# Optimization experiments

Hardware: AMD Instinct MI355X
Metric: run time of the kernel (lower is better)

Reference implementation:

```python
import jax, jax.numpy as jnp
import numpy as np

D = 128        # embed_d
L = 2          # n_layers
B = 4096       # batch of center nodes (drugs)
S = 10         # num_samples per neighbor type (hard-coded in node_het_agg)
NUM_CELLS, NUM_DRUGS, NUM_GENES = 2000, 4000, 20000
DRUG_F, GENE_F = 1024, 2048
NT = 3         # node types: cell, drug, gene


def setup_inputs() -> dict:
    key = jax.random.key(0)
    ks = jax.random.split(key, 16)
    s = 0.02
    inp = {
        # raw per-type feature tables (feature_loader / embedding table)
        "drug_feats": jax.random.normal(ks[0], (NUM_DRUGS, DRUG_F), jnp.float32),
        "gene_feats": jax.random.normal(ks[1], (NUM_GENES, GENE_F), jnp.float32),
        "cell_tab": jax.random.normal(ks[2], (NUM_CELLS, D), jnp.float32) * s,
        # feat_proj linears
        "W_drug": jax.random.normal(ks[3], (DRUG_F, D), jnp.float32) * s,
        "b_drug": jnp.zeros((D,), jnp.float32),
        "W_gene": jax.random.normal(ks[4], (GENE_F, D), jnp.float32) * s,
        "b_gene": jnp.zeros((D,), jnp.float32),
        # RnnGnnLayer params: per layer, per neighbor type, a simple tanh RNN
        "rnn_Wx": jax.random.normal(ks[5], (L, NT, D, D), jnp.float32) * s,
        "rnn_Wh": jax.random.normal(ks[6], (L, NT, D, D), jnp.float32) * s,
        "rnn_b": jnp.zeros((L, NT, D), jnp.float32),
        # per-layer attention vector over [self || candidate]
        "att_w": jax.random.normal(ks[7], (L, 2 * D), jnp.float32) * s,
        # center node ids (drug type) and pre-sampled neighbor ids per layer/type
        "center_ids": jax.random.randint(ks[8], (B,), 0, NUM_DRUGS, jnp.int32),
        "cell_neigh": jax.random.randint(ks[9], (L, B, S), 0, NUM_CELLS, jnp.int32),
        "drug_neigh": jax.random.randint(ks[10], (L, B, S), 0, NUM_DRUGS, jnp.int32),
        "gene_neigh": jax.random.randint(ks[11], (L, B, S), 0, NUM_GENES, jnp.int32),
    }
    return inp


def reference(drug_feats, gene_feats, cell_tab, W_drug, b_drug, W_gene, b_gene,
              rnn_Wx, rnn_Wh, rnn_b, att_w,
              center_ids, cell_neigh, drug_neigh, gene_neigh):
    # conteng_agg per node type: gather raw features then project to embed_d
    def emb_cell(idx):
        return cell_tab[idx]                              # [..., D]

    def emb_drug(idx):
        return drug_feats[idx] @ W_drug + b_drug          # gather [..., DRUG_F] -> [..., D]

    def emb_gene(idx):
        return gene_feats[idx] @ W_gene + b_gene

    def rnn_agg(x, Wx, Wh, b):
        # x: [B, S, D]; simple tanh RNN over the S sampled neighbors, last hidden
        def step(h, xt):
            h = jnp.tanh(xt @ Wx + h @ Wh + b)
            return h, None
        h0 = jnp.zeros((x.shape[0], Wx.shape[1]), x.dtype)
        h_last, _ = jax.lax.scan(step, h0, jnp.swapaxes(x, 0, 1))
        return h_last                                      # [B, D]

    h = emb_drug(center_ids)                               # initial center embeds [B, D]
    n_layers = rnn_Wx.shape[0]
    for l in range(n_layers):
        neigh = [(cell_neigh[l], emb_cell), (drug_neigh[l], emb_drug), (gene_neigh[l], emb_gene)]
        aggs = []
        for t, (idx, emb) in enumerate(neigh):
            x = emb(idx)                                   # [B, S, D]
            aggs.append(rnn_agg(x, rnn_Wx[l, t], rnn_Wh[l, t], rnn_b[l, t]))
        cands = jnp.stack([h] + aggs, axis=1)              # [B, 1+NT, D]
        self_b = jnp.broadcast_to(h[:, None, :], cands.shape)
        scores = jax.nn.leaky_relu(jnp.concatenate([self_b, cands], axis=-1) @ att_w[l])  # [B, 1+NT]
        alpha = jax.nn.softmax(scores, axis=1)
        h = jnp.einsum('bc,bcd->bd', alpha, cands)         # attention-weighted combine
    return h                                               # [B, D]
```

## Files before the change

kernel.cpp:

```cpp
#include <hip/hip_runtime.h>
#include <stdint.h>

#define D 128
#define Ssz 10
#define HP 136

typedef uint16_t u16;
typedef uint32_t u32;
typedef __attribute__((ext_vector_type(8))) short short8;
typedef __attribute__((ext_vector_type(4))) float f32x4;

#define AS1U32(p) ((const __attribute__((address_space(1))) u32*)(p))
#define AS3U32(p) ((__attribute__((address_space(3))) u32*)(p))

__device__ __forceinline__ u16 f2bf(float f){
  u32 x = __float_as_uint(f);
  return (u16)((x + 0x7fffu + ((x >> 16) & 1u)) >> 16);
}
__device__ __forceinline__ float bf2f(u16 u){ return __uint_as_float(((u32)u) << 16); }

__device__ __forceinline__ float ftanh(float x){
  float e = __expf(2.0f * x);
  return 1.0f - 2.0f / (e + 1.0f);
}

__global__ __launch_bounds__(256) void transpose_k(const float* __restrict__ W,
                                                   u16* __restrict__ WT, int K){
  int i = blockIdx.x * 256 + threadIdx.x;
  if (i >= K * D) return;
  int n = i / K, k = i - n * K;
  WT[i] = f2bf(W[k * D + n]);
}

__global__ __launch_bounds__(256) void transpose_b6(const float* __restrict__ W,
                                                    u16* __restrict__ WT){
  int i = blockIdx.x * 256 + threadIdx.x;
  int j = i & 16383, n = j >> 7, k = j & 127;
  WT[i] = f2bf(W[(i & ~16383) + k * D + n]);
}

__global__ __launch_bounds__(256) void cvt_bf16(const float* __restrict__ in,
                                                u16* __restrict__ out, int n2){
  int i = blockIdx.x * 256 + threadIdx.x;
  if (i >= n2) return;
  float v0 = in[2 * i], v1 = in[2 * i + 1];
  ((u32*)out)[i] = (u32)f2bf(v0) | ((u32)f2bf(v1) << 16);
}

__global__ __launch_bounds__(256) void proj_gemm(
    const float* __restrict__ feats, int K, int M,
    const u16* __restrict__ WT,
    const float* __restrict__ bias,
    u16* __restrict__ outb,
    float* __restrict__ outf)
{
  __shared__ u16 Bt[128 * 128];

  int lane = threadIdx.x & 63;
  int wave = threadIdx.x >> 6;
  int quad = lane >> 4, l16 = lane & 15;
  int m0 = blockIdx.x * 64 + wave * 16;

  int row = min(m0 + l16, M - 1);
  const float* aptr = feats + (long)row * K + quad * 8;

  int st_nrow = wave * 32 + (lane >> 4);
  int st_p    = lane & 15;

  f32x4 acc[8];
#pragma unroll
  for (int nt = 0; nt < 8; ++nt){
    float bv = bias[nt * 16 + l16];
    f32x4 t = {bv, bv, bv, bv};
    acc[nt] = t;
  }

  f32x4 afA[4][2], afB[4][2];
#pragma unroll
  for (int ks = 0; ks < 4; ++ks){
    afA[ks][0] = *(const f32x4*)(aptr + ks * 32);
    afA[ks][1] = *(const f32x4*)(aptr + ks * 32 + 4);
  }

  auto chunk_step = [&](f32x4 (&acur)[4][2], f32x4 (&anxt)[4][2], int kc) {
#pragma unroll
    for (int j = 0; j < 8; ++j){
      int n = st_nrow + j * 4;
      int c = st_p ^ (n & 15);
      const u16* g = WT + (long)n * K + kc + c * 8;
      __builtin_amdgcn_global_load_lds(AS1U32(g),
                                       AS3U32(&Bt[(wave * 8 + j) * 512]),
                                       16, 0, 0);
    }
    if (kc + 128 < K){
#pragma unroll
      for (int ks = 0; ks < 4; ++ks){
        anxt[ks][0] = *(const f32x4*)(aptr + kc + 128 + ks * 32);
        anxt[ks][1] = *(const f32x4*)(aptr + kc + 128 + ks * 32 + 4);
      }
    }
    __syncthreads();

#pragma unroll
    for (int ks = 0; ks < 4; ++ks){
      short8 a;
#pragma unroll
      for (int q = 0; q < 4; ++q){
        a[q]     = (short)f2bf(acur[ks][0][q]);
        a[4 + q] = (short)f2bf(acur[ks][1][q]);
      }
#pragma unroll
      for (int nt = 0; nt < 8; ++nt){
        int n = nt * 16 + l16;
        int p = (ks * 4 + quad) ^ l16;
        short8 b = *(const short8*)(&Bt[n * 128 + p * 8]);
        acc[nt] = __builtin_amdgcn_mfma_f32_16x16x32_bf16(a, b, acc[nt], 0, 0, 0);
      }
    }
    __syncthreads();
  };

  for (int kc = 0; kc < K; kc += 256){
    chunk_step(afA, afB, kc);
    chunk_step(afB, afA, kc + 128);
  }

#pragma unroll
  for (int nt = 0; nt < 8; ++nt){
    int col = nt * 16 + l16;
#pragma unroll
    for (int r = 0; r < 4; ++r){
      int mr = m0 + quad * 4 + r;
      if (mr < M){
        long o = (long)mr * D + col;
        if (outb) outb[o] = f2bf(acc[nt][r]);
        if (outf) outf[o] = acc[nt][r];
      }
    }
  }
}

__global__ __launch_bounds__(256) void xw_gemm(
    const u16* __restrict__ cellT, const u16* __restrict__ drugPb,
    const u16* __restrict__ genePb,
    const u16* __restrict__ WxT6,
    const float* __restrict__ bvec,
    float* __restrict__ xwb)
{
  int bx = blockIdx.x, l = blockIdx.y;
  int t, m0, M, rbase;
  const u16* tab;
  if (bx < 32)      { t = 0; m0 = bx * 64;        M = 2000;  rbase = 0;    tab = cellT; }
  else if (bx < 95) { t = 1; m0 = (bx - 32) * 64; M = 4000;  rbase = 2000; tab = drugPb; }
  else              { t = 2; m0 = (bx - 95) * 64; M = 20000; rbase = 6000; tab = genePb; }
  int mat = l * 3 + t;
  const u16* WT = WxT6 + (size_t)mat * 16384;

  int lane = threadIdx.x & 63, wave = threadIdx.x >> 6;
  int quad = lane >> 4, l16 = lane & 15;
  int mt = m0 + wave * 16;
  int mr = min(mt + l16, M - 1);

  short8 a[4];
#pragma unroll
  for (int ks = 0; ks < 4; ++ks)
    a[ks] = *(const short8*)(tab + (long)mr * D + ks * 32 + quad * 8);

  f32x4 acc[8];
#pragma unroll
  for (int nt = 0; nt < 8; ++nt){
    float bv = bvec[mat * D + nt * 16 + l16];
    f32x4 tv = {bv, bv, bv, bv};
    acc[nt] = tv;
  }
#pragma unroll
  for (int nt = 0; nt < 8; ++nt){
#pragma unroll
    for (int ks = 0; ks < 4; ++ks){
      short8 b = *(const short8*)(WT + (nt * 16 + l16) * D + ks * 32 + quad * 8);
      acc[nt] = __builtin_amdgcn_mfma_f32_16x16x32_bf16(a[ks], b, acc[nt], 0, 0, 0);
    }
  }
#pragma unroll
  for (int nt = 0; nt < 8; ++nt){
    int col = nt * 16 + l16;
#pragma unroll
    for (int r = 0; r < 4; ++r){
      int mrow = mt + quad * 4 + r;
      if (mrow < M)
        xwb[((long)l * 26000 + rbase + mrow) * D + col] = acc[nt][r];
    }
  }
}

__global__ __launch_bounds__(256) void gather_f32(
    const float* __restrict__ tab, const int* __restrict__ idx,
    float* __restrict__ out, int nrows, int ntab)
{
  int gt = blockIdx.x * 256 + threadIdx.x;
  int r = gt >> 6, c = gt & 63;
  if (r >= nrows) return;
  int row = min(max(idx[r], 0), ntab - 1);
  ((float2*)out)[(long)r * 64 + c] = ((const float2*)tab)[(long)row * 64 + c];
}

__global__ __launch_bounds__(256, 3) void rnn6_kernel(
    const float* __restrict__ xwb,
    const u16* __restrict__ WhT6,
    const int* __restrict__ cn, const int* __restrict__ dn,
    const int* __restrict__ gn,
    int b0,
    u16* __restrict__ agg, int CB)
{
  __shared__ u16 hbuf[16 * HP];

  int t = blockIdx.y, l = blockIdx.z;
  const int* idx = (t == 0) ? cn : (t == 1) ? dn : gn;
  int rbase = (t == 0) ? 0 : (t == 1) ? 2000 : 6000;
  int nmax  = (t == 0) ? 2000 : (t == 1) ? 4000 : 20000;
  const float* xw = xwb + ((size_t)l * 26000 + rbase) * D;
  const u16* WT = WhT6 + (size_t)(l * 3 + t) * 16384;

  int tid = threadIdx.x, lane = tid & 63, wave = tid >> 6;
  int quad = lane >> 4, l16 = lane & 15;
  int n0 = wave * 32;

  short8 whf[2][4];
#pragma unroll
  for (int nt = 0; nt < 2; ++nt){
    int n = n0 + nt * 16 + l16;
#pragma unroll
    for (int ks = 0; ks < 4; ++ks)
      whf[nt][ks] = *(const short8*)(WT + n * D + ks * 32 + quad * 8);
  }

  for (int i = tid; i < 16 * HP; i += 256) hbuf[i] = 0;

  int brow = blockIdx.x * 16;
  const int* ip = idx + ((size_t)l * 4096 + b0 + brow + quad * 4) * Ssz;
  long arow = ((long)(l * 3 + t) * CB + brow) * D;

  int nidA[4], nidB[4];
  float xwA[8], xwB[8];
#pragma unroll
  for (int r = 0; r < 4; ++r) nidA[r] = min(max(ip[r * Ssz], 0), nmax - 1);
#pragma unroll
  for (int r = 0; r < 4; ++r){
    const float* p = xw + (long)nidA[r] * D + n0 + l16;
    xwA[r] = p[0]; xwA[4 + r] = p[16];
  }
#pragma unroll
  for (int r = 0; r < 4; ++r) nidB[r] = min(max(ip[r * Ssz + 1], 0), nmax - 1);
  __syncthreads();

  auto step = [&](int s, float (&xwc)[8], int (&nidn)[4],
                  float (&xwn)[8], int (&nidf)[4]){
    if (s + 1 < Ssz){
#pragma unroll
      for (int r = 0; r < 4; ++r){
        const float* p = xw + (long)nidn[r] * D + n0 + l16;
        xwn[r] = p[0]; xwn[4 + r] = p[16];
      }
    }
    if (s + 2 < Ssz){
#pragma unroll
      for (int r = 0; r < 4; ++r)
        nidf[r] = min(max(ip[r * Ssz + s + 2], 0), nmax - 1);
    }
    short8 hf[4];
#pragma unroll
    for (int ks = 0; ks < 4; ++ks)
      hf[ks] = *(const short8*)(&hbuf[l16 * HP + ks * 32 + quad * 8]);
    f32x4 acc0 = {xwc[0], xwc[1], xwc[2], xwc[3]};
    f32x4 acc1 = {xwc[4], xwc[5], xwc[6], xwc[7]};
#pragma unroll
    for (int ks = 0; ks < 4; ++ks){
      acc0 = __builtin_amdgcn_mfma_f32_16x16x32_bf16(hf[ks], whf[0][ks], acc0, 0, 0, 0);
      acc1 = __builtin_amdgcn_mfma_f32_16x16x32_bf16(hf[ks], whf[1][ks], acc1, 0, 0, 0);
    }
    __syncthreads();
#pragma unroll
    for (int r = 0; r < 4; ++r){
      float v0 = ftanh(acc0[r]);
      float v1 = ftanh(acc1[r]);
      hbuf[(quad * 4 + r) * HP + n0 + l16]      = f2bf(v0);
      hbuf[(quad * 4 + r) * HP + n0 + 16 + l16] = f2bf(v1);
      if (s == Ssz - 1){
        long o = arow + (long)(quad * 4 + r) * D;
        agg[o + n0 + l16]      = f2bf(v0);
        agg[o + n0 + 16 + l16] = f2bf(v1);
      }
    }
    __syncthreads();
  };

  step(0, xwA, nidB, xwB, nidA);
  step(1, xwB, nidA, xwA, nidB);
  step(2, xwA, nidB, xwB, nidA);
  step(3, xwB, nidA, xwA, nidB);
  step(4, xwA, nidB, xwB, nidA);
  step(5, xwB, nidA, xwA, nidB);
  step(6, xwA, nidB, xwB, nidA);
  step(7, xwB, nidA, xwA, nidB);
  step(8, xwA, nidB, xwB, nidA);
  step(9, xwB, nidA, xwA, nidB);
}

__global__ __launch_bounds__(256) void att_kernel(
    const float* __restrict__ h,
    const u16* __restrict__ agg,
    const float* __restrict__ aw,
    float* __restrict__ out,
    int CB)
{
  int gt = blockIdx.x * 256 + threadIdx.x;
  int lane = gt & 63;
  int b = gt >> 6;
  int e = 2 * lane;

  float c[4][2];
  c[0][0] = h[(long)b * D + e];
  c[0][1] = h[(long)b * D + e + 1];
#pragma unroll
  for (int t = 0; t < 3; ++t){
    c[t + 1][0] = bf2f(agg[((long)t * CB + b) * D + e]);
    c[t + 1][1] = bf2f(agg[((long)t * CB + b) * D + e + 1]);
  }
  float as0 = aw[e],     as1 = aw[e + 1];
  float ac0 = aw[D + e], ac1 = aw[D + e + 1];

  float selfp = c[0][0] * as0 + c[0][1] * as1;
  float sc[4];
#pragma unroll
  for (int cc = 0; cc < 4; ++cc) sc[cc] = selfp + c[cc][0] * ac0 + c[cc][1] * ac1;
#pragma unroll
  for (int off = 32; off >= 1; off >>= 1){
#pragma unroll
    for (int cc = 0; cc < 4; ++cc) sc[cc] += __shfl_xor(sc[cc], off, 64);
  }
#pragma unroll
  for (int cc = 0; cc < 4; ++cc) sc[cc] = sc[cc] > 0.f ? sc[cc] : 0.01f * sc[cc];

  float mx = fmaxf(fmaxf(sc[0], sc[1]), fmaxf(sc[2], sc[3]));
  float ex[4], ssum = 0.f;
#pragma unroll
  for (int cc = 0; cc < 4; ++cc){ ex[cc] = expf(sc[cc] - mx); ssum += ex[cc]; }
  float o0 = 0.f, o1 = 0.f;
#pragma unroll
  for (int cc = 0; cc < 4; ++cc){
    float a = ex[cc] / ssum;
    o0 += a * c[cc][0];
    o1 += a * c[cc][1];
  }
  out[(long)b * D + e]     = o0;
  out[(long)b * D + e + 1] = o1;
}

extern "C" void kernel_launch(void* const* d_in, const int* in_sizes, int n_in,
                              void* d_out, int out_size, void* d_ws, size_t ws_size,
                              hipStream_t stream)
{
  const float* drug_feats = (const float*)d_in[0];
  const float* gene_feats = (const float*)d_in[1];
  const float* cell_tab   = (const float*)d_in[2];
  const float* W_drug     = (const float*)d_in[3];
  const float* b_drug     = (const float*)d_in[4];
  const float* W_gene     = (const float*)d_in[5];
  const float* b_gene     = (const float*)d_in[6];
  const float* rnn_Wx     = (const float*)d_in[7];
  const float* rnn_Wh     = (const float*)d_in[8];
  const float* rnn_b      = (const float*)d_in[9];
  const float* att_w      = (const float*)d_in[10];
  const int* center_ids   = (const int*)d_in[11];
  const int* cell_neigh   = (const int*)d_in[12];
  const int* drug_neigh   = (const int*)d_in[13];
  const int* gene_neigh   = (const int*)d_in[14];

  u16* ws     = (u16*)d_ws;
  u16* WdT    = ws;
  u16* WgT    = WdT + 131072;
  u16* WxT6   = WgT + 262144;
  u16* WhT6   = WxT6 + 98304;
  u16* cellT  = WhT6 + 98304;
  u16* drugPb = cellT + 256000;
  u16* genePb = drugPb + 512000;
  float* drugPf = (float*)(genePb + 2560000);
  float* xwb    = drugPf + 512000;
  u16* agg      = (u16*)(xwb + 6656000);

  int CB = 4096;
  while (CB > 64){
    size_t need = 36507648u + (size_t)1536 * CB;
    if (need <= ws_size) break;
    CB >>= 1;
  }
  float* h = (float*)d_out;

  transpose_k<<<512, 256, 0, stream>>>(W_drug, WdT, 1024);
  transpose_k<<<1024, 256, 0, stream>>>(W_gene, WgT, 2048);
  transpose_b6<<<384, 256, 0, stream>>>(rnn_Wx, WxT6);
  transpose_b6<<<384, 256, 0, stream>>>(rnn_Wh, WhT6);
  cvt_bf16<<<500, 256, 0, stream>>>(cell_tab, cellT, 2000 * 64);

  proj_gemm<<<63, 256, 0, stream>>>(drug_feats, 1024, 4000,
                                    WdT, b_drug, drugPb, drugPf);
  proj_gemm<<<313, 256, 0, stream>>>(gene_feats, 2048, 20000,
                                     WgT, b_gene, genePb, (float*)nullptr);

  xw_gemm<<<dim3(408, 2), 256, 0, stream>>>(cellT, drugPb, genePb,
                                            WxT6, rnn_b, xwb);

  for (int b0 = 0; b0 < 4096; b0 += CB){
    gather_f32<<<CB / 4, 256, 0, stream>>>(drugPf, center_ids + b0,
                                           h + (size_t)b0 * D, CB, 4000);
    rnn6_kernel<<<dim3(CB / 16, 3, 2), 256, 0, stream>>>(
        xwb, WhT6, cell_neigh, drug_neigh, gene_neigh, b0, agg, CB);

    for (int l = 0; l < 2; ++l){
      att_kernel<<<CB / 4, 256, 0, stream>>>(h + (size_t)b0 * D,
                                             agg + (size_t)l * 3 * CB * D,
                                             att_w + (size_t)l * 2 * D,
                                             h + (size_t)b0 * D, CB);
    }
  }
}
```

Before: 366.7 us.

## Fuse prep kernels, projection with Wx GEMM, and gather with attention layers

Merges the five weight/table conversion kernels into one prep kernel. The per-type Wx GEMM now runs inside the projection GEMM epilogue, reusing the accumulator tile from LDS, so the bf16 projected tables are never written or reloaded. The center gather and both attention layers are fused into one kernel, and the workspace-dependent chunking loop is dropped. This cuts launch count and global traffic, but it assumes the workspace can hold the full batch and makes the projection kernel's epilogue longer.

Measured after the change: 360.9 us. No clear change (-1.6%).

```diff
diff --git a/kernel.cpp b/kernel.cpp
--- a/kernel.cpp
+++ b/kernel.cpp
@@ -4,6 +4,7 @@
 #define D 128
 #define Ssz 10
 #define HP 136
+#define NB 4096
 
 typedef uint16_t u16;
 typedef uint32_t u32;
@@ -24,34 +25,47 @@
   return 1.0f - 2.0f / (e + 1.0f);
 }
 
-__global__ __launch_bounds__(256) void transpose_k(const float* __restrict__ W,
-                                                   u16* __restrict__ WT, int K){
+__global__ __launch_bounds__(256) void prep_kernel(
+    const float* __restrict__ W_drug, const float* __restrict__ W_gene,
+    const float* __restrict__ rnn_Wx, const float* __restrict__ rnn_Wh,
+    const float* __restrict__ cell_tab,
+    u16* __restrict__ WdT, u16* __restrict__ WgT,
+    u16* __restrict__ WxT6, u16* __restrict__ WhT6,
+    u16* __restrict__ cellT)
+{
   int i = blockIdx.x * 256 + threadIdx.x;
-  if (i >= K * D) return;
-  int n = i / K, k = i - n * K;
-  WT[i] = f2bf(W[k * D + n]);
-}
-
-__global__ __launch_bounds__(256) void transpose_b6(const float* __restrict__ W,
-                                                    u16* __restrict__ WT){
-  int i = blockIdx.x * 256 + threadIdx.x;
-  int j = i & 16383, n = j >> 7, k = j & 127;
-  WT[i] = f2bf(W[(i & ~16383) + k * D + n]);
-}
-
-__global__ __launch_bounds__(256) void cvt_bf16(const float* __restrict__ in,
-                                                u16* __restrict__ out, int n2){
-  int i = blockIdx.x * 256 + threadIdx.x;
-  if (i >= n2) return;
-  float v0 = in[2 * i], v1 = in[2 * i + 1];
-  ((u32*)out)[i] = (u32)f2bf(v0) | ((u32)f2bf(v1) << 16);
+  if (i < 131072){
+    int n = i >> 10, k = i & 1023;
+    WdT[i] = f2bf(W_drug[k * D + n]);
+  } else if (i < 393216){
+    int j = i - 131072;
+    int n = j >> 11, k = j & 2047;
+    WgT[j] = f2bf(W_gene[k * D + n]);
+  } else if (i < 491520){
+    int j = i - 393216;
+    int n = (j >> 7) & 127, k = j & 127;
+    WxT6[j] = f2bf(rnn_Wx[(j & ~16383) + k * D + n]);
+  } else if (i < 589824){
+    int j = i - 491520;
+    int n = (j >> 7) & 127, k = j & 127;
+    WhT6[j] = f2bf(rnn_Wh[(j & ~16383) + k * D + n]);
+  } else {
+    int j = i - 589824;
+    float v0 = cell_tab[2 * j], v1 = cell_tab[2 * j + 1];
+    ((u32*)cellT)[j] = (u32)f2bf(v0) | ((u32)f2bf(v1) << 16);
+  }
 }
 
 __global__ __launch_bounds__(256) void proj_gemm(
     const float* __restrict__ feats, int K, int M,
     const u16* __restrict__ WT,
     const float* __restrict__ bias,
-    u16* __restrict__ outb,
+    const u16* __restrict__ Wx0,
+    const u16* __restrict__ Wx1,
+    const float* __restrict__ rb0,
+    const float* __restrict__ rb1,
+    float* __restrict__ xw0,
+    float* __restrict__ xw1,
     float* __restrict__ outf)
 {
   __shared__ u16 Bt[128 * 128];
@@ -125,46 +139,80 @@
     chunk_step(afB, afA, kc + 128);
   }
 
-#pragma unroll
-  for (int nt = 0; nt < 8; ++nt){
-    int col = nt * 16 + l16;
-#pragma unroll
-    for (int r = 0; r < 4; ++r){
-      int mr = m0 + quad * 4 + r;
-      if (mr < M){
-        long o = (long)mr * D + col;
-        if (outb) outb[o] = f2bf(acc[nt][r]);
-        if (outf) outf[o] = acc[nt][r];
-      }
-    }
-  }
-}
-
-__global__ __launch_bounds__(256) void xw_gemm(
-    const u16* __restrict__ cellT, const u16* __restrict__ drugPb,
-    const u16* __restrict__ genePb,
+  if (outf){
+#pragma unroll
+    for (int nt = 0; nt < 8; ++nt){
+      int col = nt * 16 + l16;
+#pragma unroll
+      for (int r = 0; r < 4; ++r){
+        int mr = m0 + quad * 4 + r;
+        if (mr < M) outf[(long)mr * D + col] = acc[nt][r];
+      }
+    }
+  }
+
+  u16* Pl = Bt + wave * 2176;
+#pragma unroll
+  for (int nt = 0; nt < 8; ++nt)
+#pragma unroll
+    for (int r = 0; r < 4; ++r)
+      Pl[(quad * 4 + r) * HP + nt * 16 + l16] = f2bf(acc[nt][r]);
+  __syncthreads();
+
+  short8 paf[4];
+#pragma unroll
+  for (int ks = 0; ks < 4; ++ks)
+    paf[ks] = *(const short8*)(&Pl[l16 * HP + ks * 32 + quad * 8]);
+
+  auto xw_pass = [&](const u16* Wx, const float* rb, float* xw){
+    f32x4 ac2[8];
+#pragma unroll
+    for (int nt = 0; nt < 8; ++nt){
+      float bv = rb[nt * 16 + l16];
+      f32x4 tv = {bv, bv, bv, bv};
+      ac2[nt] = tv;
+    }
+#pragma unroll
+    for (int nt = 0; nt < 8; ++nt){
+#pragma unroll
+      for (int ks = 0; ks < 4; ++ks){
+        short8 b = *(const short8*)(Wx + (nt * 16 + l16) * D + ks * 32 + quad * 8);
+        ac2[nt] = __builtin_amdgcn_mfma_f32_16x16x32_bf16(paf[ks], b, ac2[nt], 0, 0, 0);
+      }
+    }
+#pragma unroll
+    for (int nt = 0; nt < 8; ++nt){
+      int col = nt * 16 + l16;
+#pragma unroll
+      for (int r = 0; r < 4; ++r){
+        int mr = m0 + quad * 4 + r;
+        if (mr < M) xw[(long)mr * D + col] = ac2[nt][r];
+      }
+    }
+  };
+  xw_pass(Wx0, rb0, xw0);
+  xw_pass(Wx1, rb1, xw1);
+}
+
+__global__ __launch_bounds__(256) void xw_cell(
+    const u16* __restrict__ cellT,
     const u16* __restrict__ WxT6,
     const float* __restrict__ bvec,
     float* __restrict__ xwb)
 {
-  int bx = blockIdx.x, l = blockIdx.y;
-  int t, m0, M, rbase;
-  const u16* tab;
-  if (bx < 32)      { t = 0; m0 = bx * 64;        M = 2000;  rbase = 0;    tab = cellT; }
-  else if (bx < 95) { t = 1; m0 = (bx - 32) * 64; M = 4000;  rbase = 2000; tab = drugPb; }
-  else              { t = 2; m0 = (bx - 95) * 64; M = 20000; rbase = 6000; tab = genePb; }
-  int mat = l * 3 + t;
+  int l = blockIdx.y;
+  int mat = l * 3;
   const u16* WT = WxT6 + (size_t)mat * 16384;
 
   int lane = threadIdx.x & 63, wave = threadIdx.x >> 6;
   int quad = lane >> 4, l16 = lane & 15;
-  int mt = m0 + wave * 16;
-  int mr = min(mt + l16, M - 1);
+  int mt = blockIdx.x * 64 + wave * 16;
+  int mr = min(mt + l16, 1999);
 
   short8 a[4];
 #pragma unroll
   for (int ks = 0; ks < 4; ++ks)
-    a[ks] = *(const short8*)(tab + (long)mr * D + ks * 32 + quad * 8);
+    a[ks] = *(const short8*)(cellT + (long)mr * D + ks * 32 + quad * 8);
 
   f32x4 acc[8];
 #pragma unroll
@@ -187,21 +235,10 @@
 #pragma unroll
     for (int r = 0; r < 4; ++r){
       int mrow = mt + quad * 4 + r;
-      if (mrow < M)
-        xwb[((long)l * 26000 + rbase + mrow) * D + col] = acc[nt][r];
-    }
-  }
-}
-
-__global__ __launch_bounds__(256) void gather_f32(
-    const float* __restrict__ tab, const int* __restrict__ idx,
-    float* __restrict__ out, int nrows, int ntab)
-{
-  int gt = blockIdx.x * 256 + threadIdx.x;
-  int r = gt >> 6, c = gt & 63;
-  if (r >= nrows) return;
-  int row = min(max(idx[r], 0), ntab - 1);
-  ((float2*)out)[(long)r * 64 + c] = ((const float2*)tab)[(long)row * 64 + c];
+      if (mrow < 2000)
+        xwb[((long)l * 26000 + mrow) * D + col] = acc[nt][r];
+    }
+  }
 }
 
 __global__ __launch_bounds__(256, 3) void rnn6_kernel(
@@ -209,8 +246,7 @@
     const u16* __restrict__ WhT6,
     const int* __restrict__ cn, const int* __restrict__ dn,
     const int* __restrict__ gn,
-    int b0,
-    u16* __restrict__ agg, int CB)
+    u16* __restrict__ agg)
 {
   __shared__ u16 hbuf[16 * HP];
 
@@ -237,8 +273,8 @@
   for (int i = tid; i < 16 * HP; i += 256) hbuf[i] = 0;
 
   int brow = blockIdx.x * 16;
-  const int* ip = idx + ((size_t)l * 4096 + b0 + brow + quad * 4) * Ssz;
-  long arow = ((long)(l * 3 + t) * CB + brow) * D;
+  const int* ip = idx + ((size_t)l * NB + brow + quad * 4) * Ssz;
+  long arow = ((long)(l * 3 + t) * NB + brow) * D;
 
   int nidA[4], nidB[4];
   float xwA[8], xwB[8];
@@ -306,54 +342,63 @@
   step(9, xwB, nidA, xwA, nidB);
 }
 
-__global__ __launch_bounds__(256) void att_kernel(
-    const float* __restrict__ h,
+__global__ __launch_bounds__(256) void att2_kernel(
+    const float* __restrict__ drugPf,
+    const int* __restrict__ center_ids,
     const u16* __restrict__ agg,
-    const float* __restrict__ aw,
-    float* __restrict__ out,
-    int CB)
+    const float* __restrict__ att_w,
+    float* __restrict__ out)
 {
   int gt = blockIdx.x * 256 + threadIdx.x;
   int lane = gt & 63;
   int b = gt >> 6;
   int e = 2 * lane;
 
-  float c[4][2];
-  c[0][0] = h[(long)b * D + e];
-  c[0][1] = h[(long)b * D + e + 1];
-#pragma unroll
-  for (int t = 0; t < 3; ++t){
-    c[t + 1][0] = bf2f(agg[((long)t * CB + b) * D + e]);
-    c[t + 1][1] = bf2f(agg[((long)t * CB + b) * D + e + 1]);
-  }
-  float as0 = aw[e],     as1 = aw[e + 1];
-  float ac0 = aw[D + e], ac1 = aw[D + e + 1];
-
-  float selfp = c[0][0] * as0 + c[0][1] * as1;
-  float sc[4];
-#pragma unroll
-  for (int cc = 0; cc < 4; ++cc) sc[cc] = selfp + c[cc][0] * ac0 + c[cc][1] * ac1;
-#pragma unroll
-  for (int off = 32; off >= 1; off >>= 1){
-#pragma unroll
-    for (int cc = 0; cc < 4; ++cc) sc[cc] += __shfl_xor(sc[cc], off, 64);
-  }
-#pragma unroll
-  for (int cc = 0; cc < 4; ++cc) sc[cc] = sc[cc] > 0.f ? sc[cc] : 0.01f * sc[cc];
-
-  float mx = fmaxf(fmaxf(sc[0], sc[1]), fmaxf(sc[2], sc[3]));
-  float ex[4], ssum = 0.f;
-#pragma unroll
-  for (int cc = 0; cc < 4; ++cc){ ex[cc] = expf(sc[cc] - mx); ssum += ex[cc]; }
-  float o0 = 0.f, o1 = 0.f;
-#pragma unroll
-  for (int cc = 0; cc < 4; ++cc){
-    float a = ex[cc] / ssum;
-    o0 += a * c[cc][0];
-    o1 += a * c[cc][1];
-  }
-  out[(long)b * D + e]     = o0;
-  out[(long)b * D + e + 1] = o1;
+  int row = min(max(center_ids[b], 0), 3999);
+  float h0 = drugPf[(long)row * D + e];
+  float h1 = drugPf[(long)row * D + e + 1];
+
+#pragma unroll
+  for (int l = 0; l < 2; ++l){
+    float c[4][2];
+    c[0][0] = h0; c[0][1] = h1;
+#pragma unroll
+    for (int t = 0; t < 3; ++t){
+      long o = ((long)(l * 3 + t) * NB + b) * D + e;
+      c[t + 1][0] = bf2f(agg[o]);
+      c[t + 1][1] = bf2f(agg[o + 1]);
+    }
+    const float* aw = att_w + l * 2 * D;
+    float as0 = aw[e],     as1 = aw[e + 1];
+    float ac0 = aw[D + e], ac1 = aw[D + e + 1];
+
+    float selfp = c[0][0] * as0 + c[0][1] * as1;
+    float sc[4];
+#pragma unroll
+    for (int cc = 0; cc < 4; ++cc) sc[cc] = selfp + c[cc][0] * ac0 + c[cc][1] * ac1;
+#pragma unroll
+    for (int off = 32; off >= 1; off >>= 1){
+#pragma unroll
+      for (int cc = 0; cc < 4; ++cc) sc[cc] += __shfl_xor(sc[cc], off, 64);
+    }
+#pragma unroll
+    for (int cc = 0; cc < 4; ++cc) sc[cc] = sc[cc] > 0.f ? sc[cc] : 0.01f * sc[cc];
+
+    float mx = fmaxf(fmaxf(sc[0], sc[1]), fmaxf(sc[2], sc[3]));
+    float ex[4], ssum = 0.f;
+#pragma unroll
+    for (int cc = 0; cc < 4; ++cc){ ex[cc] = expf(sc[cc] - mx); ssum += ex[cc]; }
+    float o0 = 0.f, o1 = 0.f;
+#pragma unroll
+    for (int cc = 0; cc < 4; ++cc){
+      float a = ex[cc] / ssum;
+      o0 += a * c[cc][0];
+      o1 += a * c[cc][1];
+    }
+    h0 = o0; h1 = o1;
+  }
+  out[(long)b * D + e]     = h0;
+  out[(long)b * D + e + 1] = h1;
 }
 
 extern "C" void kernel_launch(void* const* d_in, const int* in_sizes, int n_in,
@@ -382,45 +427,32 @@
   u16* WxT6   = WgT + 262144;
   u16* WhT6   = WxT6 + 98304;
   u16* cellT  = WhT6 + 98304;
-  u16* drugPb = cellT + 256000;
-  u16* genePb = drugPb + 512000;
-  float* drugPf = (float*)(genePb + 2560000);
+  float* drugPf = (float*)(cellT + 256000);
   float* xwb    = drugPf + 512000;
   u16* agg      = (u16*)(xwb + 6656000);
 
-  int CB = 4096;
-  while (CB > 64){
-    size_t need = 36507648u + (size_t)1536 * CB;
-    if (need <= ws_size) break;
-    CB >>= 1;
-  }
   float* h = (float*)d_out;
 
-  transpose_k<<<512, 256, 0, stream>>>(W_drug, WdT, 1024);
-  transpose_k<<<1024, 256, 0, stream>>>(W_gene, WgT, 2048);
-  transpose_b6<<<384, 256, 0, stream>>>(rnn_Wx, WxT6);
-  transpose_b6<<<384, 256, 0, stream>>>(rnn_Wh, WhT6);
-  cvt_bf16<<<500, 256, 0, stream>>>(cell_tab, cellT, 2000 * 64);
-
-  proj_gemm<<<63, 256, 0, stream>>>(drug_feats, 1024, 4000,
-                                    WdT, b_drug, drugPb, drugPf);
-  proj_gemm<<<313, 256, 0, stream>>>(gene_feats, 2048, 20000,
-                                     WgT, b_gene, genePb, (float*)nullptr);
-
-  xw_gemm<<<dim3(408, 2), 256, 0, stream>>>(cellT, drugPb, genePb,
-                                            WxT6, rnn_b, xwb);
-
-  for (int b0 = 0; b0 < 4096; b0 += CB){
-    gather_f32<<<CB / 4, 256, 0, stream>>>(drugPf, center_ids + b0,
-                                           h + (size_t)b0 * D, CB, 4000);
-    rnn6_kernel<<<dim3(CB / 16, 3, 2), 256, 0, stream>>>(
-        xwb, WhT6, cell_neigh, drug_neigh, gene_neigh, b0, agg, CB);
-
-    for (int l = 0; l < 2; ++l){
-      att_kernel<<<CB / 4, 256, 0, stream>>>(h + (size_t)b0 * D,
-                                             agg + (size_t)l * 3 * CB * D,
-                                             att_w + (size_t)l * 2 * D,
-                                             h + (size_t)b0 * D, CB);
-    }
-  }
-}
+  prep_kernel<<<2804, 256, 0, stream>>>(W_drug, W_gene, rnn_Wx, rnn_Wh, cell_tab,
+                                        WdT, WgT, WxT6, WhT6, cellT);
+
+  proj_gemm<<<63, 256, 0, stream>>>(drug_feats, 1024, 4000, WdT, b_drug,
+                                    WxT6 + 1 * 16384, WxT6 + 4 * 16384,
+                                    rnn_b + 1 * D,    rnn_b + 4 * D,
+                                    xwb + (size_t)(0 * 26000 + 2000) * D,
+                                    xwb + (size_t)(1 * 26000 + 2000) * D,
+                                    drugPf);
+  proj_gemm<<<313, 256, 0, stream>>>(gene_feats, 2048, 20000, WgT, b_gene,
+                                     WxT6 + 2 * 16384, WxT6 + 5 * 16384,
+                                     rnn_b + 2 * D,    rnn_b + 5 * D,
+                                     xwb + (size_t)(0 * 26000 + 6000) * D,
+                                     xwb + (size_t)(1 * 26000 + 6000) * D,
+                                     (float*)nullptr);
+
+  xw_cell<<<dim3(32, 2), 256, 0, stream>>>(cellT, WxT6, rnn_b, xwb);
+
+  rnn6_kernel<<<dim3(NB / 16, 3, 2), 256, 0, stream>>>(
+      xwb, WhT6, cell_neigh, drug_neigh, gene_neigh, agg);
+
+  att2_kernel<<<NB / 4, 256, 0, stream>>>(drugPf, center_ids, agg, att_w, h);
+}
```
